# Kernel tuning notes

Measured on AMD Instinct MI355X. Metric: run time of the kernel, lower is better.

The kernel has to match this reference:

```python
import jax, jax.numpy as jnp
import numpy as np

B, S, D, H = 2, 2048, 1024, 16
DK = D // H


def setup_inputs() -> dict:
    key = jax.random.key(0)
    ks = jax.random.split(key, 12)
    sc = 0.02
    inp = {
        "q": jax.random.normal(ks[0], (B, S, D), jnp.float32),
        "k": jax.random.normal(ks[1], (B, S, D), jnp.float32),
        "v": jax.random.normal(ks[2], (B, S, D), jnp.float32),
        "mask": jnp.ones((B, S, S), jnp.int32),
        "Wq": jax.random.normal(ks[3], (D, D), jnp.float32) * sc,
        "bq": jnp.zeros((D,), jnp.float32),
        "Wk": jax.random.normal(ks[4], (D, D), jnp.float32) * sc,
        "bk": jnp.zeros((D,), jnp.float32),
        "Wv": jax.random.normal(ks[5], (D, D), jnp.float32) * sc,
        "bv": jnp.zeros((D,), jnp.float32),
        "Wo": jax.random.normal(ks[6], (D, D), jnp.float32) * sc,
        "bo": jnp.zeros((D,), jnp.float32),
    }
    return inp


def _split_heads(x):
    # [B,S,D] -> [B,H,S,DK]
    b, s, _ = x.shape
    return x.reshape(b, s, H, DK).transpose(0, 2, 1, 3)


def reference(q, k, v, mask, Wq, bq, Wk, bk, Wv, bv, Wo, bo):
    qh = _split_heads(q @ Wq.T + bq)
    kh = _split_heads(k @ Wk.T + bk)
    vh = _split_heads(v @ Wv.T + bv)
    scale = 1.0 / jnp.sqrt(jnp.float32(DK))
    scores = jnp.einsum("bhqd,bhkd->bhqk", qh, kh) * scale  # [B,H,S,S]
    scores = jnp.where(mask[:, None, :, :] == 0, jnp.float32(-1e9), scores)
    probs = jax.nn.softmax(scores, axis=-1)  # dropout p=0.0 -> identity
    out = jnp.einsum("bhqk,bhkd->bhqd", probs, vh)  # [B,H,S,DK]
    concat = out.transpose(0, 2, 1, 3).reshape(q.shape[0], -1, D)
    return concat @ Wo.T + bo
```

## Files before the change

### kernel.cpp

```cpp
#include <hip/hip_runtime.h>
#include <stdint.h>

#define Bsz 2
#define Ssz 2048
#define Dsz 1024
#define Hsz 16
#define DKsz 64

typedef __attribute__((ext_vector_type(8))) short sh8;
typedef __attribute__((ext_vector_type(4))) float fx4;
typedef __attribute__((ext_vector_type(16))) float fx16;
typedef __attribute__((ext_vector_type(4))) unsigned ux4;

__device__ __forceinline__ unsigned short f2bf(float x) {
  uint32_t u = __builtin_bit_cast(uint32_t, x);
  uint32_t r = (u + 0x7fffu + ((u >> 16) & 1u)) >> 16;
  return (unsigned short)r;
}

__device__ __forceinline__ fx4 mfma16(sh8 a, sh8 b, fx4 c) {
  return __builtin_amdgcn_mfma_f32_16x16x32_bf16(a, b, c, 0, 0, 0);
}

__device__ __forceinline__ fx16 mfma32(sh8 a, sh8 b, fx16 c) {
  return __builtin_amdgcn_mfma_f32_32x32x16_bf16(a, b, c, 0, 0, 0);
}

__device__ __forceinline__ void g2l16(const void* g, void* l) {
  __builtin_amdgcn_global_load_lds((const __attribute__((address_space(1))) void*)g,
                                   (__attribute__((address_space(3))) void*)l, 16, 0, 0);
}

__device__ __forceinline__ float fexp2(float x) {
#if __has_builtin(__builtin_amdgcn_exp2f)
  return __builtin_amdgcn_exp2f(x);
#else
  return exp2f(x);
#endif
}

__device__ __forceinline__ unsigned cvtpk(float lo, float hi) {
  unsigned r;
  asm("v_cvt_pk_bf16_f32 %0, %1, %2" : "=v"(r) : "v"(lo), "v"(hi));
  return r;
}

__device__ __forceinline__ void plswap(unsigned& a, unsigned& b) {
  asm("v_permlane32_swap_b32 %0, %1" : "+v"(a), "+v"(b));
}

__device__ __forceinline__ void build_pa(const fx16& p, sh8& pa0, sh8& pa1) {
  unsigned w0 = cvtpk(p[0], p[1]), w1 = cvtpk(p[2], p[3]);
  unsigned w2 = cvtpk(p[4], p[5]), w3 = cvtpk(p[6], p[7]);
  unsigned w4 = cvtpk(p[8], p[9]), w5 = cvtpk(p[10], p[11]);
  unsigned w6 = cvtpk(p[12], p[13]), w7 = cvtpk(p[14], p[15]);
  plswap(w0, w2);
  plswap(w1, w3);
  ux4 u0 = {w0, w1, w2, w3};
  pa0 = __builtin_bit_cast(sh8, u0);
  plswap(w4, w6);
  plswap(w5, w7);
  ux4 u1 = {w4, w5, w6, w7};
  pa1 = __builtin_bit_cast(sh8, u1);
}

__global__ __launch_bounds__(256) void convert_kernel(
    const float* __restrict__ wq, const float* __restrict__ wk, const float* __restrict__ wv,
    const float* __restrict__ wo, const int* __restrict__ mask,
    unsigned short* __restrict__ wqb, unsigned short* __restrict__ wkb,
    unsigned short* __restrict__ wvb, unsigned short* __restrict__ wob,
    int* __restrict__ flag) {
  const int NW = Dsz * Dsz / 4;
  const int NC = 4 * NW;
  const int NM = Bsz * Ssz * Ssz / 4;
  const int total = NC + NM;
  int bad = 0;
  for (int i = blockIdx.x * blockDim.x + threadIdx.x; i < total; i += gridDim.x * blockDim.x) {
    if (i >= NC) {
      int4 m = ((const int4*)mask)[i - NC];
      if (m.x == 0 || m.y == 0 || m.z == 0 || m.w == 0) bad = 1;
      continue;
    }
    int t = i / NW, off = i - t * NW;
    const float* src = (t == 0) ? wq : ((t == 1) ? wk : ((t == 2) ? wv : wo));
    unsigned short* dst = (t == 0) ? wqb : ((t == 1) ? wkb : ((t == 2) ? wvb : wob));
    float4 x = ((const float4*)src)[off];
    ushort4 o;
    o.x = f2bf(x.x); o.y = f2bf(x.y); o.z = f2bf(x.z); o.w = f2bf(x.w);
    ((ushort4*)dst)[off] = o;
  }
  if (bad) atomicAnd(flag, 0);
}

__global__ void flag_init_kernel(int* flag) {
  if (threadIdx.x == 0 && blockIdx.x == 0) flag[0] = 1;
}

__global__ __launch_bounds__(256) void proj_qkv_kernel(
    const float* __restrict__ qf, const float* __restrict__ kf, const float* __restrict__ vf,
    const unsigned short* __restrict__ wqb, const unsigned short* __restrict__ wkb,
    const unsigned short* __restrict__ wvb,
    const float* __restrict__ bq, const float* __restrict__ bk, const float* __restrict__ bv,
    unsigned short* __restrict__ qh, unsigned short* __restrict__ kh,
    unsigned short* __restrict__ vt) {
  __shared__ __align__(16) unsigned short SMEM[17408];
  unsigned short* Ts = SMEM;
  const int z = blockIdx.z;
  const float* X = (z == 0) ? qf : ((z == 1) ? kf : vf);
  const unsigned short* W = (z == 0) ? wqb : ((z == 1) ? wkb : wvb);
  const float* bias = (z == 0) ? bq : ((z == 1) ? bk : bv);
  const int m0 = blockIdx.x * 128, n0 = blockIdx.y * 128;
  const int tid = threadIdx.x, lane = tid & 63, wid = tid >> 6;
  const int wm = wid >> 1, wn = wid & 1;
  const int c = lane & 15, g = lane >> 4;
  fx4 acc[4][4] = {};
  const int NSTEP = Dsz / 32;

  float4 rA0[4], rA1[4];

  auto LOADA = [&](int t, float4* r) {
    const int k0 = t * 32;
#pragma unroll
    for (int i = 0; i < 4; i++) {
      int c4 = i * 256 + tid;
      r[i] = *(const float4*)(X + (size_t)(m0 + (c4 >> 3)) * Dsz + k0 + (c4 & 7) * 4);
    }
  };
  auto WRITEA = [&](const float4* r, int buf) {
    unsigned short* dst = SMEM + buf * 4096;
#pragma unroll
    for (int i = 0; i < 4; i++) {
      int c4 = i * 256 + tid;
      uint2 w;
      w.x = cvtpk(r[i].x, r[i].y);
      w.y = cvtpk(r[i].z, r[i].w);
      *(uint2*)&dst[(c4 >> 3) * 32 + (c4 & 7) * 4] = w;
    }
  };
  auto G2LB = [&](int t, int buf) {
    const int k0 = t * 32;
    unsigned short* dst = SMEM + 8192 + buf * 4096;
#pragma unroll
    for (int i = 0; i < 2; i++) {
      int e = i * 256 + tid;
      g2l16(W + (size_t)(n0 + (e >> 2)) * Dsz + k0 + (e & 3) * 8,
            (char*)dst + (size_t)(i * 256 + wid * 64) * 16);
    }
  };
  auto COMPUTE = [&](int buf) {
    const unsigned short* A_ = SMEM + buf * 4096;
    const unsigned short* B_ = SMEM + 8192 + buf * 4096;
    sh8 af[4], bfr[4];
#pragma unroll
    for (int m = 0; m < 4; m++)
      af[m] = *(const sh8*)&A_[(wm * 64 + m * 16 + c) * 32 + g * 8];
#pragma unroll
    for (int n = 0; n < 4; n++)
      bfr[n] = *(const sh8*)&B_[(wn * 64 + n * 16 + c) * 32 + g * 8];
#pragma unroll
    for (int m = 0; m < 4; m++)
#pragma unroll
      for (int n = 0; n < 4; n++)
        acc[m][n] = mfma16(af[m], bfr[n], acc[m][n]);
  };

  LOADA(0, rA0);
  G2LB(0, 0);
  LOADA(1, rA1);
  WRITEA(rA0, 0);
  asm volatile("s_waitcnt vmcnt(4)" ::: "memory");
  __builtin_amdgcn_s_barrier();
  asm volatile("" ::: "memory");

#pragma unroll 1
  for (int t = 0; t < NSTEP; t += 2) {
    G2LB(t + 1, 1);
    if (t + 2 < NSTEP) LOADA(t + 2, rA0);
    COMPUTE(0);
    WRITEA(rA1, 1);
    if (t + 2 < NSTEP)
      asm volatile("s_waitcnt vmcnt(4)" ::: "memory");
    else
      asm volatile("s_waitcnt vmcnt(0)" ::: "memory");
    __builtin_amdgcn_s_barrier();
    asm volatile("" ::: "memory");
    if (t + 2 < NSTEP) {
      G2LB(t + 2, 0);
      if (t + 3 < NSTEP) LOADA(t + 3, rA1);
      COMPUTE(1);
      WRITEA(rA0, 0);
      if (t + 3 < NSTEP)
        asm volatile("s_waitcnt vmcnt(4)" ::: "memory");
      else
        asm volatile("s_waitcnt vmcnt(0)" ::: "memory");
      __builtin_amdgcn_s_barrier();
      asm volatile("" ::: "memory");
    } else {
      COMPUTE(1);
    }
  }
  __syncthreads();

  const float CE = 0.18033688011112042f;
  if (z < 2) {
    unsigned short* O = (z == 0) ? qh : kh;
    const float sc = (z == 0) ? CE : 1.0f;
#pragma unroll
    for (int n = 0; n < 4; n++) {
      int nl = wn * 64 + n * 16 + c;
      float bj = bias[n0 + nl];
#pragma unroll
      for (int m = 0; m < 4; m++)
#pragma unroll
        for (int r = 0; r < 4; r++) {
          int ml = wm * 64 + m * 16 + g * 4 + r;
          Ts[ml * 136 + nl] = f2bf((acc[m][n][r] + bj) * sc);
        }
    }
    __syncthreads();
#pragma unroll
    for (int it = 0; it < 8; it++) {
      int ch = it * 256 + tid;
      int row = ch >> 4, off = ch & 15;
      sh8 dv = *(const sh8*)&Ts[row * 136 + off * 8];
      int i = m0 + row;
      int b = i >> 11, s = i & 2047;
      int j = n0 + off * 8;
      int h = j >> 6, dk = j & 63;
      *(sh8*)&O[(((size_t)(b * Hsz + h) * Ssz + s) << 6) + dk] = dv;
    }
  } else {
#pragma unroll
    for (int n = 0; n < 4; n++) {
      int nl = wn * 64 + n * 16 + c;
      float bj = bias[n0 + nl];
#pragma unroll
      for (int m = 0; m < 4; m++)
#pragma unroll
        for (int r = 0; r < 4; r++) {
          int ml = wm * 64 + m * 16 + g * 4 + r;
          Ts[nl * 136 + ml] = f2bf(acc[m][n][r] + bj);
        }
    }
    __syncthreads();
    int b = m0 >> 11, sbase = m0 & 2047;
#pragma unroll
    for (int it = 0; it < 8; it++) {
      int ch = it * 256 + tid;
      int row = ch >> 4, off = ch & 15;
      sh8 dv = *(const sh8*)&Ts[row * 136 + off * 8];
      int j = n0 + row;
      int h = j >> 6, dk = j & 63;
      *(sh8*)&vt[(size_t)((b * Hsz + h) * DKsz + dk) * Ssz + sbase + off * 8] = dv;
    }
  }
}

__global__ __launch_bounds__(512, 4) void attn_kernel(
    const unsigned short* __restrict__ qh, const unsigned short* __restrict__ kh,
    const unsigned short* __restrict__ vt, const int* __restrict__ mask,
    const int* __restrict__ flag, unsigned short* __restrict__ concat) {
  __shared__ __align__(16) unsigned short SM[2][2][2][4096];
  const int tid = threadIdx.x, lane = tid & 63, wid = tid >> 6;
  const int grp = wid >> 2, w4 = wid & 3;
  const int fid = blockIdx.y * gridDim.x + blockIdx.x;
  const int logical = (fid & 7) * 64 + (fid >> 3);
  const int bh = logical >> 4, qblk = logical & 15;
  const int b = bh >> 4, h = bh & 15;
  const int q0 = qblk * 128 + w4 * 32;
  const int c = lane & 31, hi = lane >> 5;
  const int cs = c & 7;
  const int kvbase = grp * (Ssz / 2);
  const unsigned short* Qb = qh + ((size_t)bh * Ssz + q0) * DKsz;
  const unsigned short* Kb = kh + (size_t)bh * Ssz * DKsz;
  const unsigned short* Vb = vt + (size_t)bh * DKsz * Ssz;
  const int ch0 = w4 * 128 + lane;
  const int ch1 = ch0 + 64;
  const int r0 = ch0 >> 3, sl0 = (ch0 & 7) ^ (r0 & 7);
  const int r1 = ch1 >> 3, sl1 = (ch1 & 7) ^ (r1 & 7);
  const int koff0 = r0 * DKsz + sl0 * 8, koff1 = r1 * DKsz + sl1 * 8;
  const size_t voff0 = (size_t)r0 * Ssz + sl0 * 8, voff1 = (size_t)r1 * Ssz + sl1 * 8;

  sh8 qf[4];
#pragma unroll
  for (int ks = 0; ks < 4; ks++)
    qf[ks] = *(const sh8*)&Qb[(size_t)c * DKsz + ks * 16 + hi * 8];
  const bool allones = (flag[0] != 0);
  float lsum = 0.f;
  fx16 o0 = {}, o1 = {};

  auto STAGE = [&](int bufi, int kv0) {
    const unsigned short* ksrc = Kb + (size_t)kv0 * DKsz;
    char* kdst = (char*)&SM[0][grp][bufi][0] + w4 * 2048;
    g2l16(ksrc + koff0, kdst);
    g2l16(ksrc + koff1, kdst + 1024);
    const unsigned short* vsrc = Vb + kv0;
    char* vdst = (char*)&SM[1][grp][bufi][0] + w4 * 2048;
    g2l16(vsrc + voff0, vdst);
    g2l16(vsrc + voff1, vdst + 1024);
  };

  const int NT = (Ssz / 2) / 64;
  STAGE(0, kvbase);
  asm volatile("s_waitcnt vmcnt(0)" ::: "memory");
  __builtin_amdgcn_s_barrier();
  asm volatile("" ::: "memory");

  for (int t = 0; t < NT; ++t) {
    const int cur = t & 1;
    const int kv0 = kvbase + t * 64;
    if (t + 1 < NT) STAGE(cur ^ 1, kv0 + 64);
    const unsigned short* Kt = &SM[0][grp][cur][0];
    const unsigned short* Vt = &SM[1][grp][cur][0];
    fx16 s0 = {}, s1 = {};
    __builtin_amdgcn_s_setprio(1);
#pragma unroll
    for (int ks = 0; ks < 4; ks++) {
      int sl = (2 * ks + hi) ^ cs;
      sh8 ka = *(const sh8*)&Kt[(c * 8 + sl) * 8];
      sh8 kb2 = *(const sh8*)&Kt[((32 + c) * 8 + sl) * 8];
      s0 = mfma32(ka, qf[ks], s0);
      s1 = mfma32(kb2, qf[ks], s1);
    }
    __builtin_amdgcn_s_setprio(0);
    if (!allones) {
      const int* mrow = mask + ((size_t)b * Ssz + (q0 + c)) * Ssz + kv0;
#pragma unroll
      for (int r = 0; r < 16; r++) {
        int kv = (r & 3) + 8 * (r >> 2) + 4 * hi;
        if (mrow[kv] == 0) s0[r] = -1e9f;
        if (mrow[32 + kv] == 0) s1[r] = -1e9f;
      }
    }
    fx16 p0v, p1v;
#pragma unroll
    for (int r = 0; r < 16; r++) {
      p0v[r] = fexp2(s0[r]);
      p1v[r] = fexp2(s1[r]);
    }
    sh8 pa[4];
    build_pa(p0v, pa[0], pa[1]);
    build_pa(p1v, pa[2], pa[3]);
    __builtin_amdgcn_s_setprio(1);
#pragma unroll
    for (int ks = 0; ks < 4; ks++) {
      int sl = (2 * ks + hi) ^ cs;
      sh8 v0f = *(const sh8*)&Vt[(c * 8 + sl) * 8];
      sh8 v1f = *(const sh8*)&Vt[((32 + c) * 8 + sl) * 8];
      o0 = mfma32(v0f, pa[ks], o0);
      o1 = mfma32(v1f, pa[ks], o1);
    }
    __builtin_amdgcn_s_setprio(0);
    float sm[16];
#pragma unroll
    for (int r = 0; r < 16; r++) sm[r] = p0v[r] + p1v[r];
#pragma unroll
    for (int w = 8; w >= 1; w >>= 1)
#pragma unroll
      for (int r = 0; r < w; r++) sm[r] += sm[r + w];
    lsum += sm[0];
    asm volatile("s_waitcnt vmcnt(0)" ::: "memory");
    __builtin_amdgcn_s_barrier();
    asm volatile("" ::: "memory");
  }

  float* CB = (float*)&SM[0][0][0][0];
  float* CBl = CB + 4 * 32 * 68;
  if (grp == 1) {
#pragma unroll
    for (int k4 = 0; k4 < 4; k4++) {
      fx4 a = {o0[4 * k4], o0[4 * k4 + 1], o0[4 * k4 + 2], o0[4 * k4 + 3]};
      *(fx4*)&CB[(w4 * 32 + c) * 68 + 8 * k4 + 4 * hi] = a;
      fx4 bvv = {o1[4 * k4], o1[4 * k4 + 1], o1[4 * k4 + 2], o1[4 * k4 + 3]};
      *(fx4*)&CB[(w4 * 32 + c) * 68 + 32 + 8 * k4 + 4 * hi] = bvv;
    }
    CBl[w4 * 64 + hi * 32 + c] = lsum;
  }
  __syncthreads();
  if (grp == 0) {
#pragma unroll
    for (int k4 = 0; k4 < 4; k4++) {
      fx4 a = *(const fx4*)&CB[(w4 * 32 + c) * 68 + 8 * k4 + 4 * hi];
      o0[4 * k4] += a[0]; o0[4 * k4 + 1] += a[1]; o0[4 * k4 + 2] += a[2]; o0[4 * k4 + 3] += a[3];
      fx4 bvv = *(const fx4*)&CB[(w4 * 32 + c) * 68 + 32 + 8 * k4 + 4 * hi];
      o1[4 * k4] += bvv[0]; o1[4 * k4 + 1] += bvv[1]; o1[4 * k4 + 2] += bvv[2]; o1[4 * k4 + 3] += bvv[3];
    }
    lsum += CBl[w4 * 64 + hi * 32 + c];
    lsum += __shfl_xor(lsum, 32);
    float linv = 1.0f / lsum;
    unsigned short* Ob = concat + ((size_t)b * Ssz + q0 + c) * Dsz + h * DKsz;
#pragma unroll
    for (int rg = 0; rg < 4; rg++) {
      ushort4 w;
      w.x = f2bf(o0[rg * 4 + 0] * linv);
      w.y = f2bf(o0[rg * 4 + 1] * linv);
      w.z = f2bf(o0[rg * 4 + 2] * linv);
      w.w = f2bf(o0[rg * 4 + 3] * linv);
      *(ushort4*)&Ob[8 * rg + 4 * hi] = w;
      ushort4 w2;
      w2.x = f2bf(o1[rg * 4 + 0] * linv);
      w2.y = f2bf(o1[rg * 4 + 1] * linv);
      w2.z = f2bf(o1[rg * 4 + 2] * linv);
      w2.w = f2bf(o1[rg * 4 + 3] * linv);
      *(ushort4*)&Ob[32 + 8 * rg + 4 * hi] = w2;
    }
  }
}

__global__ __launch_bounds__(256) void outproj_kernel(
    const unsigned short* __restrict__ Xc, const unsigned short* __restrict__ wob,
    const float* __restrict__ bo, float* __restrict__ out) {
  __shared__ __align__(16) unsigned short As[128 * 32];
  __shared__ __align__(16) unsigned short Bs[128 * 32];
  const int m0 = blockIdx.x * 128, n0 = blockIdx.y * 128;
  const int tid = threadIdx.x, lane = tid & 63, wid = tid >> 6;
  const int wm = wid >> 1, wn = wid & 1;
  const int c = lane & 15, g = lane >> 4;
  fx4 acc[4][4] = {};
  for (int k0 = 0; k0 < Dsz; k0 += 32) {
#pragma unroll
    for (int i = 0; i < 2; i++) {
      int e = i * 256 + tid;
      g2l16(Xc + (size_t)(m0 + (e >> 2)) * Dsz + k0 + (e & 3) * 8,
            (char*)As + (size_t)(i * 256 + wid * 64) * 16);
      g2l16(wob + (size_t)(n0 + (e >> 2)) * Dsz + k0 + (e & 3) * 8,
            (char*)Bs + (size_t)(i * 256 + wid * 64) * 16);
    }
    __syncthreads();
    sh8 af[4], bfr[4];
#pragma unroll
    for (int m = 0; m < 4; m++)
      af[m] = *(const sh8*)&As[(wm * 64 + m * 16 + c) * 32 + g * 8];
#pragma unroll
    for (int n = 0; n < 4; n++)
      bfr[n] = *(const sh8*)&Bs[(wn * 64 + n * 16 + c) * 32 + g * 8];
#pragma unroll
    for (int m = 0; m < 4; m++)
#pragma unroll
      for (int n = 0; n < 4; n++)
        acc[m][n] = mfma16(af[m], bfr[n], acc[m][n]);
    __syncthreads();
  }
#pragma unroll
  for (int n = 0; n < 4; n++) {
    int j = n0 + wn * 64 + n * 16 + c;
    float bj = bo[j];
#pragma unroll
    for (int m = 0; m < 4; m++)
#pragma unroll
      for (int r = 0; r < 4; r++) {
        int i = m0 + wm * 64 + m * 16 + g * 4 + r;
        out[(size_t)i * Dsz + j] = acc[m][n][r] + bj;
      }
  }
}

extern "C" void kernel_launch(void* const* d_in, const int* in_sizes, int n_in,
                              void* d_out, int out_size, void* d_ws, size_t ws_size,
                              hipStream_t stream) {
  const float* q = (const float*)d_in[0];
  const float* k = (const float*)d_in[1];
  const float* v = (const float*)d_in[2];
  const int* mask = (const int*)d_in[3];
  const float* Wq = (const float*)d_in[4];
  const float* bq = (const float*)d_in[5];
  const float* Wk = (const float*)d_in[6];
  const float* bk = (const float*)d_in[7];
  const float* Wv = (const float*)d_in[8];
  const float* bv = (const float*)d_in[9];
  const float* Wo = (const float*)d_in[10];
  const float* bo = (const float*)d_in[11];
  float* out = (float*)d_out;
  char* ws = (char*)d_ws;
  const size_t MB = 1 << 20;
  unsigned short* wqb = (unsigned short*)(ws + 0 * MB);
  unsigned short* wkb = (unsigned short*)(ws + 2 * MB);
  unsigned short* wvb = (unsigned short*)(ws + 4 * MB);
  unsigned short* wob = (unsigned short*)(ws + 6 * MB);
  unsigned short* qhp = (unsigned short*)(ws + 8 * MB);
  unsigned short* khp = (unsigned short*)(ws + 16 * MB);
  unsigned short* vtp = (unsigned short*)(ws + 24 * MB);
  unsigned short* cc  = (unsigned short*)(ws + 32 * MB);
  int* flag = (int*)(ws + 40 * MB);

  hipLaunchKernelGGL(flag_init_kernel, dim3(1), dim3(64), 0, stream, flag);
  hipLaunchKernelGGL(convert_kernel, dim3(1024), dim3(256), 0, stream,
                     Wq, Wk, Wv, Wo, mask, wqb, wkb, wvb, wob, flag);
  hipLaunchKernelGGL(proj_qkv_kernel, dim3(32, 8, 3), dim3(256), 0, stream,
                     q, k, v, wqb, wkb, wvb, bq, bk, bv, qhp, khp, vtp);
  hipLaunchKernelGGL(attn_kernel, dim3(16, 32), dim3(512), 0, stream,
                     qhp, khp, vtp, mask, flag, cc);
  hipLaunchKernelGGL(outproj_kernel, dim3(32, 8), dim3(256), 0, stream,
                     cc, wob, bo, out);
}
```

Baseline: 144.6 us.

## Triple-buffer weight tiles in LDS to prefetch two k-steps ahead

The QKV projection GEMM now keeps three LDS buffers for the bf16 weight tiles and rotates through them, issuing the weight load two k-steps ahead instead of one. The activation tile stays double-buffered through registers. The goal is to hide more of the global-to-LDS latency behind the MFMA work. In exchange the kernel uses more shared memory, which can lower occupancy. At the tail, the fixed vmcnt(6) wait no longer covers the last weight loads, so those LDS reads could race with loads still in flight.

```diff
diff --git a/kernel.cpp b/kernel.cpp
--- a/kernel.cpp
+++ b/kernel.cpp
@@ -103,7 +103,7 @@
     const float* __restrict__ bq, const float* __restrict__ bk, const float* __restrict__ bv,
     unsigned short* __restrict__ qh, unsigned short* __restrict__ kh,
     unsigned short* __restrict__ vt) {
-  __shared__ __align__(16) unsigned short SMEM[17408];
+  __shared__ __align__(16) unsigned short SMEM[20480];
   unsigned short* Ts = SMEM;
   const int z = blockIdx.z;
   const float* X = (z == 0) ? qf : ((z == 1) ? kf : vf);
@@ -147,9 +147,9 @@
             (char*)dst + (size_t)(i * 256 + wid * 64) * 16);
     }
   };
-  auto COMPUTE = [&](int buf) {
-    const unsigned short* A_ = SMEM + buf * 4096;
-    const unsigned short* B_ = SMEM + 8192 + buf * 4096;
+  auto COMPUTE = [&](int bufA, int bufB) {
+    const unsigned short* A_ = SMEM + bufA * 4096;
+    const unsigned short* B_ = SMEM + 8192 + bufB * 4096;
     sh8 af[4], bfr[4];
 #pragma unroll
     for (int m = 0; m < 4; m++)
@@ -166,37 +166,43 @@
 
   LOADA(0, rA0);
   G2LB(0, 0);
+  G2LB(1, 1);
   LOADA(1, rA1);
   WRITEA(rA0, 0);
-  asm volatile("s_waitcnt vmcnt(4)" ::: "memory");
+  asm volatile("s_waitcnt vmcnt(6)" ::: "memory");
   __builtin_amdgcn_s_barrier();
   asm volatile("" ::: "memory");
 
+  int bB = 0;
 #pragma unroll 1
   for (int t = 0; t < NSTEP; t += 2) {
-    G2LB(t + 1, 1);
-    if (t + 2 < NSTEP) LOADA(t + 2, rA0);
-    COMPUTE(0);
-    WRITEA(rA1, 1);
-    if (t + 2 < NSTEP)
-      asm volatile("s_waitcnt vmcnt(4)" ::: "memory");
-    else
-      asm volatile("s_waitcnt vmcnt(0)" ::: "memory");
-    __builtin_amdgcn_s_barrier();
-    asm volatile("" ::: "memory");
-    if (t + 2 < NSTEP) {
-      G2LB(t + 2, 0);
-      if (t + 3 < NSTEP) LOADA(t + 3, rA1);
-      COMPUTE(1);
-      WRITEA(rA0, 0);
-      if (t + 3 < NSTEP)
-        asm volatile("s_waitcnt vmcnt(4)" ::: "memory");
-      else
-        asm volatile("s_waitcnt vmcnt(0)" ::: "memory");
+    {
+      int b2 = bB + 2; if (b2 >= 3) b2 -= 3;
+      if (t + 2 < NSTEP) {
+        G2LB(t + 2, b2);
+        LOADA(t + 2, rA0);
+      }
+      COMPUTE(0, bB);
+      WRITEA(rA1, 1);
+      asm volatile("s_waitcnt vmcnt(6)" ::: "memory");
       __builtin_amdgcn_s_barrier();
       asm volatile("" ::: "memory");
-    } else {
-      COMPUTE(1);
+      bB = bB + 1; if (bB >= 3) bB -= 3;
+    }
+    {
+      int b2 = bB + 2; if (b2 >= 3) b2 -= 3;
+      if (t + 3 < NSTEP) {
+        G2LB(t + 3, b2);
+        LOADA(t + 3, rA1);
+      }
+      COMPUTE(1, bB);
+      if (t + 2 < NSTEP) {
+        WRITEA(rA0, 0);
+        asm volatile("s_waitcnt vmcnt(6)" ::: "memory");
+        __builtin_amdgcn_s_barrier();
+        asm volatile("" ::: "memory");
+      }
+      bB = bB + 1; if (bB >= 3) bB -= 3;
     }
   }
   __syncthreads();
```

Measured after the change: 150.2 us. +3.9%, slower.
